# Kernel tuning notes

Hardware: AMD Instinct MI355X
Metric: run time of the kernel (lower is better)

The kernel has to match this reference:

```python
import jax, jax.numpy as jnp
import numpy as np

H = 16          # num attention heads
KVH = 4         # num key/value heads
HD = 128        # head dim
EPS = 1e-6


def _rms_norm(x, w):
    norm = jax.lax.rsqrt(jnp.mean(x * x, axis=-1, keepdims=True) + EPS)
    return x * norm * w


def setup_inputs() -> dict:
    key = jax.random.key(0)
    ks = jax.random.split(key, 12)
    B, L, D, F = 2, 2048, 2048, 5632
    KD = KVH * HD  # 512
    s = lambda fan_in: 1.0 / np.sqrt(fan_in)
    return {
        "x": jax.random.normal(ks[0], (B, L, D), jnp.float32),
        "ln1_w": jnp.ones((D,), jnp.float32),
        "q_w": jax.random.normal(ks[1], (D, D), jnp.float32) * s(D),
        "q_b": jax.random.normal(ks[2], (D,), jnp.float32) * 0.02,
        "k_w": jax.random.normal(ks[3], (KD, D), jnp.float32) * s(D),
        "k_b": jax.random.normal(ks[4], (KD,), jnp.float32) * 0.02,
        "v_w": jax.random.normal(ks[5], (KD, D), jnp.float32) * s(D),
        "v_b": jax.random.normal(ks[6], (KD,), jnp.float32) * 0.02,
        "o_w": jax.random.normal(ks[7], (D, D), jnp.float32) * s(D),
        "ln2_w": jnp.ones((D,), jnp.float32),
        "gate_w": jax.random.normal(ks[8], (F, D), jnp.float32) * s(D),
        "up_w": jax.random.normal(ks[9], (F, D), jnp.float32) * s(D),
        "down_w": jax.random.normal(ks[10], (D, F), jnp.float32) * s(F),
    }


def reference(x, ln1_w, q_w, q_b, k_w, k_b, v_w, v_b, o_w, ln2_w,
              gate_w, up_w, down_w):
    B, L, D = x.shape
    rep = H // KVH

    # --- attention sub-block ---
    h = _rms_norm(x, ln1_w)
    q = (h @ q_w.T + q_b).reshape(B, L, H, HD).transpose(0, 2, 1, 3)     # [B,H,L,hd]
    k = (h @ k_w.T + k_b).reshape(B, L, KVH, HD).transpose(0, 2, 1, 3)   # [B,KVH,L,hd]
    v = (h @ v_w.T + v_b).reshape(B, L, KVH, HD).transpose(0, 2, 1, 3)
    # torch .repeat tiles the whole kv-head axis: [kv0..kv3, kv0..kv3, ...]
    k = jnp.tile(k, (1, rep, 1, 1))                                      # [B,H,L,hd]
    v = jnp.tile(v, (1, rep, 1, 1))

    scale = HD ** -0.5
    scores = jnp.einsum('bhqd,bhkd->bhqk', q, k) * scale                 # [B,H,L,L]
    causal = jnp.tril(jnp.ones((L, L), bool))
    scores = jnp.where(causal, scores, -jnp.inf)
    attn = jax.nn.softmax(scores, axis=-1)
    out = jnp.einsum('bhqk,bhkd->bhqd', attn, v)                         # [B,H,L,hd]
    out = out.transpose(0, 2, 1, 3).reshape(B, L, H * HD)
    x = x + out @ o_w.T

    # --- SwiGLU MLP sub-block ---
    h2 = _rms_norm(x, ln2_w)
    mlp = (jax.nn.silu(h2 @ gate_w.T) * (h2 @ up_w.T)) @ down_w.T
    return x + mlp
```

## Files before the change

### kernel.cpp

```cpp
#include <hip/hip_runtime.h>

typedef unsigned short u16;
typedef __attribute__((ext_vector_type(8))) short s8v;
typedef __attribute__((ext_vector_type(4))) float f4v;

#define MFMA16(a, b, c) __builtin_amdgcn_mfma_f32_16x16x32_bf16(a, b, c, 0, 0, 0)

#define B_    2
#define L_    2048
#define D_    2048
#define H_    16
#define KVH_  4
#define HD_   128
#define F_    5632
#define FC_   1408
#define MTOK  (B_ * L_)
#define NEG_BIG (-1e30f)
#define SCL2E 0.127517416f

__device__ __forceinline__ float b2f(u16 h) {
  union { float f; unsigned u; } v; v.u = ((unsigned)h) << 16; return v.f;
}
__device__ __forceinline__ u16 f2b(float f) {
  union { float f; unsigned u; } v; v.f = f;
  unsigned r = v.u + 0x7FFFu + ((v.u >> 16) & 1u);
  return (u16)(r >> 16);
}
__device__ __forceinline__ s8v ld8(const u16* p) { return *reinterpret_cast<const s8v*>(p); }
__device__ __forceinline__ void st8(u16* p, s8v v) { *reinterpret_cast<s8v*>(p) = v; }
__device__ __forceinline__ void gld16(const u16* g, u16* l) {
  __builtin_amdgcn_global_load_lds((const __attribute__((address_space(1))) void*)g,
                                   (__attribute__((address_space(3))) void*)l, 16, 0, 0);
}

__global__ __launch_bounds__(256) void conv_k(const float* __restrict__ src,
                                              u16* __restrict__ dst, int n8) {
  int i = blockIdx.x * 256 + threadIdx.x;
  const int stride = gridDim.x * 256;
  for (; i < n8; i += stride) {
    const float* p = src + (size_t)i * 8;
    float4 a = *(const float4*)p, b = *(const float4*)(p + 4);
    float f[8] = {a.x, a.y, a.z, a.w, b.x, b.y, b.z, b.w};
    s8v o;
#pragma unroll
    for (int j = 0; j < 8; ++j) o[j] = (short)f2b(f[j]);
    st8(dst + (size_t)i * 8, o);
  }
}

__global__ __launch_bounds__(256) void catbias_k(const float* __restrict__ qb,
                                                 const float* __restrict__ kb,
                                                 const float* __restrict__ vb,
                                                 float* __restrict__ o) {
  int i = blockIdx.x * 256 + threadIdx.x;
  float v;
  if (i < 2048) v = qb[i];
  else if (i < 2560) v = kb[i - 2048];
  else v = vb[i - 2560];
  o[i] = v;
}

__global__ __launch_bounds__(256) void rmsnorm_k(const float* __restrict__ x,
                                                 const float* __restrict__ w,
                                                 u16* __restrict__ out) {
  const int row = blockIdx.x, t = threadIdx.x;
  const float* xr = x + (size_t)row * D_ + t * 8;
  float4 a = *(const float4*)(xr);
  float4 b = *(const float4*)(xr + 4);
  float f[8] = {a.x, a.y, a.z, a.w, b.x, b.y, b.z, b.w};
  float ss = 0.f;
#pragma unroll
  for (int j = 0; j < 8; ++j) ss += f[j] * f[j];
#pragma unroll
  for (int m = 1; m < 64; m <<= 1) ss += __shfl_xor(ss, m);
  __shared__ float red[4];
  if ((t & 63) == 0) red[t >> 6] = ss;
  __syncthreads();
  float tot = red[0] + red[1] + red[2] + red[3];
  float inv = rsqrtf(tot * (1.f / D_) + 1e-6f);
  float4 wa = *(const float4*)(w + t * 8);
  float4 wb = *(const float4*)(w + t * 8 + 4);
  float wf[8] = {wa.x, wa.y, wa.z, wa.w, wb.x, wb.y, wb.z, wb.w};
  s8v o;
#pragma unroll
  for (int j = 0; j < 8; ++j) o[j] = (short)f2b(f[j] * inv * wf[j]);
  st8(out + (size_t)row * D_ + t * 8, o);
}

template <bool C_F32>
__global__ __launch_bounds__(256) void gemm_bb(const u16* __restrict__ A, int lda,
                                               const u16* __restrict__ W, int ldw,
                                               const float* __restrict__ bias,
                                               const float* resid,
                                               const u16* gatein,
                                               void* Cv,
                                               int N, int K) {
  __shared__ __align__(16) u16 As[3][128 * 32];
  __shared__ __align__(16) u16 Bs[3][128 * 32];
  const int t = threadIdx.x;
  const int l = t & 63, w = t >> 6;
  const int lr = l & 15, lg = l >> 4;
  const int total = gridDim.x;
  const int qd = total >> 3, rr = total & 7;
  const int xc = blockIdx.x & 7, xi = blockIdx.x >> 3;
  const int pos = xc * qd + (xc < rr ? xc : rr) + xi;
  const int m0 = (pos & 31) * 128;
  const int n0 = (pos >> 5) * 128;
  const int wm = (w >> 1) * 64, wn = (w & 1) * 64;
  const int sr = t >> 2;
  const int sc = (((t & 3) ^ ((t >> 3) & 3)) * 8);
  const u16* Ag0 = A + (size_t)(m0 + sr) * lda + sc;
  const u16* Ag1 = A + (size_t)(m0 + sr + 64) * lda + sc;
  const u16* Wg0 = W + (size_t)(n0 + sr) * ldw + sc;
  const u16* Wg1 = W + (size_t)(n0 + sr + 64) * ldw + sc;

  auto stage = [&](int buf, int koff) {
    gld16(Ag0 + koff, &As[buf][w * 512]);
    gld16(Ag1 + koff, &As[buf][2048 + w * 512]);
    gld16(Wg0 + koff, &Bs[buf][w * 512]);
    gld16(Wg1 + koff, &Bs[buf][2048 + w * 512]);
  };

  const f4v zero4 = {0.f, 0.f, 0.f, 0.f};
  f4v acc[4][4];
#pragma unroll
  for (int i = 0; i < 4; ++i)
#pragma unroll
    for (int j = 0; j < 4; ++j) acc[i][j] = zero4;

  const int xq = (lr >> 1) & 3;
  const int cofA = (lg ^ xq) * 8;

  stage(0, 0);
  if (K > 32) stage(1, 32);
  int cur = 0;
  for (int k0 = 0; k0 < K; k0 += 32) {
    if (k0 + 32 < K) asm volatile("s_waitcnt vmcnt(4)" ::: "memory");
    else             asm volatile("s_waitcnt vmcnt(0)" ::: "memory");
    __builtin_amdgcn_s_barrier();
    if (k0 + 64 < K) {
      int nb = cur + 2; if (nb >= 3) nb -= 3;
      stage(nb, k0 + 64);
    }
    s8v af[4], bf[4];
#pragma unroll
    for (int i = 0; i < 4; ++i) {
      af[i] = ld8(&As[cur][(wm + i * 16 + lr) * 32 + cofA]);
      bf[i] = ld8(&Bs[cur][(wn + i * 16 + lr) * 32 + cofA]);
    }
    __builtin_amdgcn_s_setprio(1);
#pragma unroll
    for (int i = 0; i < 4; ++i)
#pragma unroll
      for (int j = 0; j < 4; ++j)
        acc[i][j] = MFMA16(af[i], bf[j], acc[i][j]);
    __builtin_amdgcn_s_setprio(0);
    ++cur; if (cur == 3) cur = 0;
  }
#pragma unroll
  for (int j = 0; j < 4; ++j) {
    const int col = n0 + wn + j * 16 + lr;
    const float bv = bias ? bias[col] : 0.f;
#pragma unroll
    for (int i = 0; i < 4; ++i) {
      const int row = m0 + wm + i * 16 + lg * 4;
#pragma unroll
      for (int r = 0; r < 4; ++r) {
        float vv = acc[i][j][r] + bv;
        size_t off = (size_t)(row + r) * N + col;
        if (gatein) {
          float gf = b2f(gatein[off]);
          vv *= gf / (1.f + __expf(-gf));
        }
        if (resid) vv += resid[off];
        if (C_F32) ((float*)Cv)[off] = vv;
        else       ((u16*)Cv)[off]   = f2b(vv);
      }
    }
  }
}

template <bool C_F32>
__global__ __launch_bounds__(256) void gemm_nt(const u16* __restrict__ A, int lda,
                                               const float* __restrict__ W, int ldw,
                                               const float* __restrict__ bias,
                                               const float* resid,
                                               const u16* gatein,
                                               void* Cv,
                                               int M, int N, int K) {
  __shared__ __align__(16) u16 As[128 * 32];
  __shared__ __align__(16) u16 Bs[128 * 32];
  const int t = threadIdx.x;
  const int l = t & 63, w = t >> 6;
  const int lr = l & 15, lg = l >> 4;
  const int m0 = blockIdx.y * 128, n0 = blockIdx.x * 128;
  const int wm = (w >> 1) * 64, wn = (w & 1) * 64;
  const int sr = t >> 2, sc = (t & 3) * 8;
  const u16* Ag0 = A + (size_t)(m0 + sr) * lda + sc;
  const u16* Ag1 = A + (size_t)(m0 + sr + 64) * lda + sc;
  const float* Wg0 = W + (size_t)(n0 + sr) * ldw + sc;
  const float* Wg1 = W + (size_t)(n0 + sr + 64) * ldw + sc;

  const f4v zero4 = {0.f, 0.f, 0.f, 0.f};
  f4v acc[4][4];
#pragma unroll
  for (int i = 0; i < 4; ++i)
#pragma unroll
    for (int j = 0; j < 4; ++j) acc[i][j] = zero4;

  for (int k0 = 0; k0 < K; k0 += 32) {
    s8v a0 = ld8(Ag0 + k0), a1 = ld8(Ag1 + k0);
    float4 w0a = *(const float4*)(Wg0 + k0), w0b = *(const float4*)(Wg0 + k0 + 4);
    float4 w1a = *(const float4*)(Wg1 + k0), w1b = *(const float4*)(Wg1 + k0 + 4);
    float wf0[8] = {w0a.x, w0a.y, w0a.z, w0a.w, w0b.x, w0b.y, w0b.z, w0b.w};
    float wf1[8] = {w1a.x, w1a.y, w1a.z, w1a.w, w1b.x, w1b.y, w1b.z, w1b.w};
    s8v b0, b1;
#pragma unroll
    for (int j = 0; j < 8; ++j) { b0[j] = (short)f2b(wf0[j]); b1[j] = (short)f2b(wf1[j]); }
    __syncthreads();
    st8(&As[sr * 32 + sc], a0);
    st8(&As[(sr + 64) * 32 + sc], a1);
    st8(&Bs[sr * 32 + sc], b0);
    st8(&Bs[(sr + 64) * 32 + sc], b1);
    __syncthreads();
    s8v af[4], bf[4];
#pragma unroll
    for (int i = 0; i < 4; ++i) {
      af[i] = ld8(&As[(wm + i * 16 + lr) * 32 + lg * 8]);
      bf[i] = ld8(&Bs[(wn + i * 16 + lr) * 32 + lg * 8]);
    }
#pragma unroll
    for (int i = 0; i < 4; ++i)
#pragma unroll
      for (int j = 0; j < 4; ++j)
        acc[i][j] = MFMA16(af[i], bf[j], acc[i][j]);
  }
#pragma unroll
  for (int j = 0; j < 4; ++j) {
    const int col = n0 + wn + j * 16 + lr;
    const float bv = bias ? bias[col] : 0.f;
#pragma unroll
    for (int i = 0; i < 4; ++i) {
      const int row = m0 + wm + i * 16 + lg * 4;
#pragma unroll
      for (int r = 0; r < 4; ++r) {
        float vv = acc[i][j][r] + bv;
        size_t off = (size_t)(row + r) * N + col;
        if (gatein) {
          float gf = b2f(gatein[off]);
          vv *= gf / (1.f + __expf(-gf));
        }
        if (resid) vv += resid[off];
        if (C_F32) ((float*)Cv)[off] = vv;
        else       ((u16*)Cv)[off]   = f2b(vv);
      }
    }
  }
}

__global__ __launch_bounds__(256) void transpose_v(const u16* __restrict__ V, int ldv,
                                                   u16* __restrict__ VT) {
  __shared__ u16 tile[64][72];
  const int t = threadIdx.x;
  const int tok0 = blockIdx.x * 64;
  const int hd0 = blockIdx.y * 64;
  const int bk = blockIdx.z;
  const int b = bk >> 2, kvh = bk & 3;
#pragma unroll
  for (int c = 0; c < 16; ++c) {
    int idx = t + c * 256;
    int tok = idx >> 6, hd = idx & 63;
    tile[tok][hd] = V[(size_t)(b * L_ + tok0 + tok) * ldv + kvh * 128 + hd0 + hd];
  }
  __syncthreads();
#pragma unroll
  for (int c = 0; c < 16; ++c) {
    int idx = t + c * 256;
    int tok = idx & 63, hd = idx >> 6;
    VT[(size_t)(bk * 128 + hd0 + hd) * L_ + tok0 + tok] = tile[tok][hd];
  }
}

__global__ __launch_bounds__(256) void attn_k(const u16* __restrict__ Q, int ldq,
                                              const u16* __restrict__ Kx, int ldk,
                                              const u16* __restrict__ VT,
                                              u16* __restrict__ O) {
  __shared__ __align__(16) u16 KtB[2][64 * 128];
  __shared__ __align__(16) u16 VtB[2][128 * 64];
  __shared__ __align__(16) u16 Pb[4 * 16 * 72];
  const int t = threadIdx.x, l = t & 63, w = t >> 6;
  const int lr = l & 15, lg = l >> 4;
  const int bh = blockIdx.y, b = bh >> 4, h = bh & 15, kvh = h & 3;
  const int qt = (int)gridDim.x - 1 - blockIdx.x;
  const int q0 = qt * 64;
  const int ktmax = qt;
  const f4v zero4 = {0.f, 0.f, 0.f, 0.f};

  const int kxr = t >> 4;
  const int kxc = (t & 15) ^ (kxr & 7);
  const int vxr = t >> 3;
  const int vxc = (t & 7) ^ (vxr & 7);
  const u16* Kg = Kx + (size_t)(b * L_) * ldk + kvh * 128;
  const u16* Vg = VT + (size_t)((b * 4 + kvh) * 128) * L_;

  auto stage = [&](int ktile, int bufi) {
#pragma unroll
    for (int c = 0; c < 4; ++c)
      gld16(Kg + (size_t)(ktile * 64 + c * 16 + kxr) * ldk + kxc * 8,
            &KtB[bufi][c * 2048 + w * 512]);
#pragma unroll
    for (int c = 0; c < 4; ++c)
      gld16(Vg + (size_t)(c * 32 + vxr) * L_ + ktile * 64 + vxc * 8,
            &VtB[bufi][c * 2048 + w * 512]);
  };

  s8v qf[4];
#pragma unroll
  for (int kf = 0; kf < 4; ++kf)
    qf[kf] = ld8(Q + (size_t)(b * L_ + q0 + w * 16 + lr) * ldq +
                 h * 128 + kf * 32 + lg * 8);

  float mrow[4], srow[4];
  f4v oacc[8];
#pragma unroll
  for (int r = 0; r < 4; ++r) { mrow[r] = NEG_BIG; srow[r] = 0.f; }
#pragma unroll
  for (int n = 0; n < 8; ++n) oacc[n] = zero4;
  u16* Pw = Pb + w * 16 * 72;

  int cur = 0;
  stage(0, 0);
  asm volatile("s_waitcnt vmcnt(0)" ::: "memory");
  __syncthreads();

  for (int kt = 0; kt <= ktmax; ++kt) {
    if (kt < ktmax) stage(kt + 1, cur ^ 1);

    f4v s[4];
#pragma unroll
    for (int nf = 0; nf < 4; ++nf) s[nf] = zero4;
    __builtin_amdgcn_s_setprio(1);
#pragma unroll
    for (int nf = 0; nf < 4; ++nf)
#pragma unroll
      for (int kf = 0; kf < 4; ++kf) {
        s8v bfr = ld8(&KtB[cur][(nf * 16 + lr) * 128 +
                                ((kf * 4 + lg) ^ (lr & 7)) * 8]);
        s[nf] = MFMA16(qf[kf], bfr, s[nf]);
      }
    __builtin_amdgcn_s_setprio(0);

    const bool needmask = (kt == ktmax);
#pragma unroll
    for (int nf = 0; nf < 4; ++nf)
#pragma unroll
      for (int r = 0; r < 4; ++r) {
        float vv = s[nf][r] * SCL2E;
        if (needmask) {
          int key = kt * 64 + nf * 16 + lr;
          int qr = q0 + w * 16 + lg * 4 + r;
          if (key > qr) vv = NEG_BIG;
        }
        s[nf][r] = vv;
      }

    float tm[4];
#pragma unroll
    for (int r = 0; r < 4; ++r) {
      float m = fmaxf(fmaxf(s[0][r], s[1][r]), fmaxf(s[2][r], s[3][r]));
#pragma unroll
      for (int msk = 1; msk < 16; msk <<= 1) m = fmaxf(m, __shfl_xor(m, msk));
      tm[r] = m;
    }
    float al[4], rs[4];
#pragma unroll
    for (int r = 0; r < 4; ++r) {
      float mn = fmaxf(mrow[r], tm[r]);
      al[r] = exp2f(mrow[r] - mn);
      mrow[r] = mn;
      rs[r] = 0.f;
    }
#pragma unroll
    for (int nf = 0; nf < 4; ++nf)
#pragma unroll
      for (int r = 0; r < 4; ++r) {
        float p = exp2f(s[nf][r] - mrow[r]);
        rs[r] += p;
        Pw[(lg * 4 + r) * 72 + nf * 16 + lr] = f2b(p);
      }
#pragma unroll
    for (int r = 0; r < 4; ++r) {
#pragma unroll
      for (int msk = 1; msk < 16; msk <<= 1) rs[r] += __shfl_xor(rs[r], msk);
      srow[r] = srow[r] * al[r] + rs[r];
    }
#pragma unroll
    for (int n = 0; n < 8; ++n)
#pragma unroll
      for (int r = 0; r < 4; ++r) oacc[n][r] *= al[r];

    s8v pa[2];
#pragma unroll
    for (int k2 = 0; k2 < 2; ++k2)
      pa[k2] = ld8(&Pw[lr * 72 + k2 * 32 + lg * 8]);
    __builtin_amdgcn_s_setprio(1);
#pragma unroll
    for (int n = 0; n < 8; ++n)
#pragma unroll
      for (int k2 = 0; k2 < 2; ++k2) {
        s8v vb = ld8(&VtB[cur][(n * 16 + lr) * 64 +
                               ((k2 * 4 + lg) ^ (lr & 7)) * 8]);
        oacc[n] = MFMA16(pa[k2], vb, oacc[n]);
      }
    __builtin_amdgcn_s_setprio(0);

    asm volatile("s_waitcnt vmcnt(0)" ::: "memory");
    __syncthreads();
    cur ^= 1;
  }

#pragma unroll
  for (int r = 0; r < 4; ++r) {
    float inv = 1.f / srow[r];
#pragma unroll
    for (int n = 0; n < 8; ++n) {
      size_t off = (size_t)(b * L_ + q0 + w * 16 + lg * 4 + r) * 2048 +
                   h * 128 + n * 16 + lr;
      O[off] = f2b(oacc[n][r] * inv);
    }
  }
}

extern "C" void kernel_launch(void* const* d_in, const int* in_sizes, int n_in,
                              void* d_out, int out_size, void* d_ws, size_t ws_size,
                              hipStream_t stream) {
  const float* x    = (const float*)d_in[0];
  const float* ln1w = (const float*)d_in[1];
  const float* qw   = (const float*)d_in[2];
  const float* qb   = (const float*)d_in[3];
  const float* kw   = (const float*)d_in[4];
  const float* kb   = (const float*)d_in[5];
  const float* vw   = (const float*)d_in[6];
  const float* vbi  = (const float*)d_in[7];
  const float* ow   = (const float*)d_in[8];
  const float* ln2w = (const float*)d_in[9];
  const float* gw   = (const float*)d_in[10];
  const float* uw   = (const float*)d_in[11];
  const float* dw   = (const float*)d_in[12];
  float* out = (float*)d_out;

  char* ws = (char*)d_ws;
  u16* h    = (u16*)(ws);
  u16* kbuf = (u16*)(ws + (16ull << 20));
  u16* vbuf = (u16*)(ws + (20ull << 20));
  u16* vt   = (u16*)(ws + (24ull << 20));
  u16* g    = (u16*)(ws + (16ull << 20));
  u16* qscr = (u16*)d_out;

  dim3 blk(256);
  const bool big = ws_size >= 119537664ull;

  rmsnorm_k<<<MTOK, blk, 0, stream>>>(x, ln1w, h);

  if (big) {
    u16* wp = (u16*)(ws + (28ull << 20));
    u16* wq = wp;
    u16* wk = wq + 4194304;
    u16* wv = wk + 1048576;
    u16* wo = wv + 1048576;
    u16* wg = wo + 4194304;
    u16* wu = wg + 11534336;
    u16* wd = wu + 11534336;
    conv_k<<<2048, blk, 0, stream>>>(qw, wq, 4194304 / 8);
    conv_k<<<512, blk, 0, stream>>>(kw, wk, 1048576 / 8);
    conv_k<<<512, blk, 0, stream>>>(vw, wv, 1048576 / 8);
    conv_k<<<2048, blk, 0, stream>>>(ow, wo, 4194304 / 8);
    conv_k<<<2048, blk, 0, stream>>>(gw, wg, 11534336 / 8);
    conv_k<<<2048, blk, 0, stream>>>(uw, wu, 11534336 / 8);
    conv_k<<<2048, blk, 0, stream>>>(dw, wd, 11534336 / 8);

    float* biasc = (float*)(ws + (16ull << 20));
    catbias_k<<<12, blk, 0, stream>>>(qb, kb, vbi, biasc);

    u16* qkv = (u16*)d_out;
    gemm_bb<false><<<768, blk, 0, stream>>>(h, D_, wq, D_, biasc, nullptr, nullptr,
                                            qkv, 3072, D_);
    transpose_v<<<dim3(32, 2, 8), blk, 0, stream>>>(qkv + 2560, 3072, vt);
    attn_k<<<dim3(32, 32), blk, 0, stream>>>(qkv, 3072, qkv + 2048, 3072, vt, h);
    gemm_bb<true><<<512, blk, 0, stream>>>(h, D_, wo, D_, nullptr, x, nullptr,
                                           d_out, 2048, D_);
    rmsnorm_k<<<MTOK, blk, 0, stream>>>(out, ln2w, h);
    for (int fc = 0; fc < 4; ++fc) {
      const u16* gwc = wg + (size_t)fc * FC_ * D_;
      const u16* uwc = wu + (size_t)fc * FC_ * D_;
      const u16* dwc = wd + (size_t)fc * FC_;
      gemm_bb<false><<<352, blk, 0, stream>>>(h, D_, gwc, D_, nullptr, nullptr,
                                              nullptr, g, FC_, D_);
      gemm_bb<false><<<352, blk, 0, stream>>>(h, D_, uwc, D_, nullptr, nullptr,
                                              g, g, FC_, D_);
      gemm_bb<true><<<512, blk, 0, stream>>>(g, FC_, dwc, F_, nullptr, out,
                                             nullptr, d_out, 2048, FC_);
    }
  } else {
    gemm_nt<false><<<dim3(16, 32), blk, 0, stream>>>(h, D_, qw, D_, qb, nullptr, nullptr,
                                                     qscr, MTOK, 2048, 2048);
    gemm_nt<false><<<dim3(4, 32), blk, 0, stream>>>(h, D_, kw, D_, kb, nullptr, nullptr,
                                                    kbuf, MTOK, 512, 2048);
    gemm_nt<false><<<dim3(4, 32), blk, 0, stream>>>(h, D_, vw, D_, vbi, nullptr, nullptr,
                                                    vbuf, MTOK, 512, 2048);
    transpose_v<<<dim3(32, 2, 8), blk, 0, stream>>>(vbuf, 512, vt);
    attn_k<<<dim3(32, 32), blk, 0, stream>>>(qscr, 2048, kbuf, 512, vt, h);
    gemm_nt<true><<<dim3(16, 32), blk, 0, stream>>>(h, D_, ow, D_, nullptr, x, nullptr,
                                                    d_out, MTOK, 2048, 2048);
    rmsnorm_k<<<MTOK, blk, 0, stream>>>(out, ln2w, h);
    for (int fc = 0; fc < 4; ++fc) {
      const float* gwc = gw + (size_t)fc * FC_ * D_;
      const float* uwc = uw + (size_t)fc * FC_ * D_;
      const float* dwc = dw + (size_t)fc * FC_;
      gemm_nt<false><<<dim3(11, 32), blk, 0, stream>>>(h, D_, gwc, D_, nullptr, nullptr,
                                                       nullptr, g, MTOK, FC_, 2048);
      gemm_nt<false><<<dim3(11, 32), blk, 0, stream>>>(h, D_, uwc, D_, nullptr, nullptr,
                                                       g, g, MTOK, FC_, 2048);
      gemm_nt<true><<<dim3(16, 32), blk, 0, stream>>>(g, FC_, dwc, F_, nullptr, out,
                                                      nullptr, d_out, MTOK, 2048, FC_);
    }
  }
}
```

Measured before the change: 1.304 ms.

## Use 256x256 GEMM tiles with 512 threads and fuse gate/up projections

Reworks the bf16 GEMM to 256x256 output tiles per 512-thread block with K-step 64 and double buffering in place of the 128x128 triple-buffered version. Gate and up weights are interleaved per chunk, so one GEMM produces both and a separate SiLU-multiply kernel combines them in place. The aim is more operand reuse per byte of LDS/global traffic and fewer launches. The trade-offs are far fewer blocks (128-192) relative to the CU count, heavier register and LDS use per block, and an extra elementwise pass over the gate/up buffer.

```diff
diff --git a/kernel.cpp b/kernel.cpp
--- a/kernel.cpp
+++ b/kernel.cpp
@@ -60,6 +60,25 @@
   o[i] = v;
 }
 
+__global__ __launch_bounds__(256) void silumul_k(u16* __restrict__ gu, int n8) {
+  int i = blockIdx.x * 256 + threadIdx.x;
+  const int stride = gridDim.x * 256;
+  for (; i < n8; i += stride) {
+    int row = i / 176, c = i - row * 176;
+    u16* gp = gu + (size_t)row * 2816 + c * 8;
+    s8v a = ld8(gp);
+    s8v b = ld8(gp + 1408);
+    s8v o;
+#pragma unroll
+    for (int j = 0; j < 8; ++j) {
+      float gf = b2f((u16)a[j]);
+      float uf = b2f((u16)b[j]);
+      o[j] = (short)f2b(gf / (1.f + __expf(-gf)) * uf);
+    }
+    st8(gp, o);
+  }
+}
+
 __global__ __launch_bounds__(256) void rmsnorm_k(const float* __restrict__ x,
                                                  const float* __restrict__ w,
                                                  u16* __restrict__ out) {
@@ -88,90 +107,88 @@
 }
 
 template <bool C_F32>
-__global__ __launch_bounds__(256) void gemm_bb(const u16* __restrict__ A, int lda,
+__global__ __launch_bounds__(512) void gemm_bb(const u16* __restrict__ A, int lda,
                                                const u16* __restrict__ W, int ldw,
                                                const float* __restrict__ bias,
                                                const float* resid,
-                                               const u16* gatein,
-                                               void* Cv,
-                                               int N, int K) {
-  __shared__ __align__(16) u16 As[3][128 * 32];
-  __shared__ __align__(16) u16 Bs[3][128 * 32];
+                                               void* Cv, int ldc, int K) {
+  __shared__ __align__(16) u16 As[2][256 * 64];
+  __shared__ __align__(16) u16 Bs[2][256 * 64];
   const int t = threadIdx.x;
   const int l = t & 63, w = t >> 6;
   const int lr = l & 15, lg = l >> 4;
-  const int total = gridDim.x;
-  const int qd = total >> 3, rr = total & 7;
-  const int xc = blockIdx.x & 7, xi = blockIdx.x >> 3;
-  const int pos = xc * qd + (xc < rr ? xc : rr) + xi;
-  const int m0 = (pos & 31) * 128;
-  const int n0 = (pos >> 5) * 128;
-  const int wm = (w >> 1) * 64, wn = (w & 1) * 64;
-  const int sr = t >> 2;
-  const int sc = (((t & 3) ^ ((t >> 3) & 3)) * 8);
-  const u16* Ag0 = A + (size_t)(m0 + sr) * lda + sc;
-  const u16* Ag1 = A + (size_t)(m0 + sr + 64) * lda + sc;
-  const u16* Wg0 = W + (size_t)(n0 + sr) * ldw + sc;
-  const u16* Wg1 = W + (size_t)(n0 + sr + 64) * ldw + sc;
-
+  const int pos = (blockIdx.x & 7) * ((int)gridDim.x >> 3) + (blockIdx.x >> 3);
+  const int m0 = (pos & 15) * 256;
+  const int n0 = (pos >> 4) * 256;
+  const int wm = (w >> 2) * 128, wn = (w & 3) * 64;
+
+  const int srow = w * 8 + (l >> 3);
+  const int cXor = ((t & 7) ^ ((t >> 3) & 7)) * 8;
+  const u16* Ag[4];
+  const u16* Wg[4];
+#pragma unroll
+  for (int li = 0; li < 4; ++li) {
+    Ag[li] = A + (size_t)(m0 + li * 64 + srow) * lda + cXor;
+    Wg[li] = W + (size_t)(n0 + li * 64 + srow) * ldw + cXor;
+  }
   auto stage = [&](int buf, int koff) {
-    gld16(Ag0 + koff, &As[buf][w * 512]);
-    gld16(Ag1 + koff, &As[buf][2048 + w * 512]);
-    gld16(Wg0 + koff, &Bs[buf][w * 512]);
-    gld16(Wg1 + koff, &Bs[buf][2048 + w * 512]);
+#pragma unroll
+    for (int li = 0; li < 4; ++li) {
+      gld16(Ag[li] + koff, &As[buf][(li * 64 + w * 8) * 64]);
+      gld16(Wg[li] + koff, &Bs[buf][(li * 64 + w * 8) * 64]);
+    }
   };
 
   const f4v zero4 = {0.f, 0.f, 0.f, 0.f};
-  f4v acc[4][4];
-#pragma unroll
-  for (int i = 0; i < 4; ++i)
+  f4v acc[8][4];
+#pragma unroll
+  for (int i = 0; i < 8; ++i)
 #pragma unroll
     for (int j = 0; j < 4; ++j) acc[i][j] = zero4;
 
-  const int xq = (lr >> 1) & 3;
-  const int cofA = (lg ^ xq) * 8;
-
+  const int NT = K >> 6;
   stage(0, 0);
-  if (K > 32) stage(1, 32);
-  int cur = 0;
-  for (int k0 = 0; k0 < K; k0 += 32) {
-    if (k0 + 32 < K) asm volatile("s_waitcnt vmcnt(4)" ::: "memory");
-    else             asm volatile("s_waitcnt vmcnt(0)" ::: "memory");
+  for (int tt = 0; tt < NT; ++tt) {
+    if (tt + 1 < NT) {
+      stage((tt + 1) & 1, (tt + 1) * 64);
+      asm volatile("s_waitcnt vmcnt(8)" ::: "memory");
+    } else {
+      asm volatile("s_waitcnt vmcnt(0)" ::: "memory");
+    }
     __builtin_amdgcn_s_barrier();
-    if (k0 + 64 < K) {
-      int nb = cur + 2; if (nb >= 3) nb -= 3;
-      stage(nb, k0 + 64);
-    }
-    s8v af[4], bf[4];
-#pragma unroll
-    for (int i = 0; i < 4; ++i) {
-      af[i] = ld8(&As[cur][(wm + i * 16 + lr) * 32 + cofA]);
-      bf[i] = ld8(&Bs[cur][(wn + i * 16 + lr) * 32 + cofA]);
-    }
-    __builtin_amdgcn_s_setprio(1);
-#pragma unroll
-    for (int i = 0; i < 4; ++i)
+    const int cur = tt & 1;
+#pragma unroll
+    for (int kk = 0; kk < 2; ++kk) {
+      const int cof = ((kk * 4 + lg) ^ (lr & 7)) * 8;
+      s8v af[8], bf[4];
+#pragma unroll
+      for (int i = 0; i < 8; ++i)
+        af[i] = ld8(&As[cur][(wm + i * 16 + lr) * 64 + cof]);
 #pragma unroll
       for (int j = 0; j < 4; ++j)
-        acc[i][j] = MFMA16(af[i], bf[j], acc[i][j]);
-    __builtin_amdgcn_s_setprio(0);
-    ++cur; if (cur == 3) cur = 0;
-  }
+        bf[j] = ld8(&Bs[cur][(wn + j * 16 + lr) * 64 + cof]);
+      __builtin_amdgcn_s_setprio(1);
+#pragma unroll
+      for (int i = 0; i < 8; ++i)
+#pragma unroll
+        for (int j = 0; j < 4; ++j)
+          acc[i][j] = MFMA16(af[i], bf[j], acc[i][j]);
+      __builtin_amdgcn_s_setprio(0);
+    }
+    __builtin_amdgcn_s_barrier();
+  }
+
 #pragma unroll
   for (int j = 0; j < 4; ++j) {
     const int col = n0 + wn + j * 16 + lr;
     const float bv = bias ? bias[col] : 0.f;
 #pragma unroll
-    for (int i = 0; i < 4; ++i) {
+    for (int i = 0; i < 8; ++i) {
       const int row = m0 + wm + i * 16 + lg * 4;
 #pragma unroll
       for (int r = 0; r < 4; ++r) {
         float vv = acc[i][j][r] + bv;
-        size_t off = (size_t)(row + r) * N + col;
-        if (gatein) {
-          float gf = b2f(gatein[off]);
-          vv *= gf / (1.f + __expf(-gf));
-        }
+        size_t off = (size_t)(row + r) * ldc + col;
         if (resid) vv += resid[off];
         if (C_F32) ((float*)Cv)[off] = vv;
         else       ((u16*)Cv)[off]   = f2b(vv);
@@ -468,38 +485,42 @@
     u16* wk = wq + 4194304;
     u16* wv = wk + 1048576;
     u16* wo = wv + 1048576;
-    u16* wg = wo + 4194304;
-    u16* wu = wg + 11534336;
-    u16* wd = wu + 11534336;
+    u16* wgu = wo + 4194304;
+    u16* wd = wgu + 23068672;
     conv_k<<<2048, blk, 0, stream>>>(qw, wq, 4194304 / 8);
     conv_k<<<512, blk, 0, stream>>>(kw, wk, 1048576 / 8);
     conv_k<<<512, blk, 0, stream>>>(vw, wv, 1048576 / 8);
     conv_k<<<2048, blk, 0, stream>>>(ow, wo, 4194304 / 8);
-    conv_k<<<2048, blk, 0, stream>>>(gw, wg, 11534336 / 8);
-    conv_k<<<2048, blk, 0, stream>>>(uw, wu, 11534336 / 8);
+    for (int c = 0; c < 4; ++c) {
+      conv_k<<<1024, blk, 0, stream>>>(gw + (size_t)c * FC_ * D_,
+                                       wgu + (size_t)c * 2816 * 2048,
+                                       FC_ * D_ / 8);
+      conv_k<<<1024, blk, 0, stream>>>(uw + (size_t)c * FC_ * D_,
+                                       wgu + (size_t)c * 2816 * 2048 + FC_ * D_,
+                                       FC_ * D_ / 8);
+    }
     conv_k<<<2048, blk, 0, stream>>>(dw, wd, 11534336 / 8);
 
     float* biasc = (float*)(ws + (16ull << 20));
     catbias_k<<<12, blk, 0, stream>>>(qb, kb, vbi, biasc);
 
     u16* qkv = (u16*)d_out;
-    gemm_bb<false><<<768, blk, 0, stream>>>(h, D_, wq, D_, biasc, nullptr, nullptr,
+    gemm_bb<false><<<192, 512, 0, stream>>>(h, D_, wq, D_, biasc, nullptr,
                                             qkv, 3072, D_);
     transpose_v<<<dim3(32, 2, 8), blk, 0, stream>>>(qkv + 2560, 3072, vt);
     attn_k<<<dim3(32, 32), blk, 0, stream>>>(qkv, 3072, qkv + 2048, 3072, vt, h);
-    gemm_bb<true><<<512, blk, 0, stream>>>(h, D_, wo, D_, nullptr, x, nullptr,
+    gemm_bb<true><<<128, 512, 0, stream>>>(h, D_, wo, D_, nullptr, x,
                                            d_out, 2048, D_);
     rmsnorm_k<<<MTOK, blk, 0, stream>>>(out, ln2w, h);
+    u16* gu = (u16*)(ws + (16ull << 20));
     for (int fc = 0; fc < 4; ++fc) {
-      const u16* gwc = wg + (size_t)fc * FC_ * D_;
-      const u16* uwc = wu + (size_t)fc * FC_ * D_;
+      const u16* wguc = wgu + (size_t)fc * 2816 * 2048;
       const u16* dwc = wd + (size_t)fc * FC_;
-      gemm_bb<false><<<352, blk, 0, stream>>>(h, D_, gwc, D_, nullptr, nullptr,
-                                              nullptr, g, FC_, D_);
-      gemm_bb<false><<<352, blk, 0, stream>>>(h, D_, uwc, D_, nullptr, nullptr,
-                                              g, g, FC_, D_);
-      gemm_bb<true><<<512, blk, 0, stream>>>(g, FC_, dwc, F_, nullptr, out,
-                                             nullptr, d_out, 2048, FC_);
+      gemm_bb<false><<<176, 512, 0, stream>>>(h, D_, wguc, D_, nullptr, nullptr,
+                                              gu, 2816, D_);
+      silumul_k<<<2048, blk, 0, stream>>>(gu, MTOK * 176);
+      gemm_bb<true><<<128, 512, 0, stream>>>(gu, 2816, dwc, F_, nullptr, out,
+                                             d_out, 2048, FC_);
     }
   } else {
     gemm_nt<false><<<dim3(16, 32), blk, 0, stream>>>(h, D_, qw, D_, qb, nullptr, nullptr,
```

Result: faster. 1.250 ms (-4.1%).
